# Kernel tuning notes

Hardware: AMD Instinct MI355X
Metric: run time of the kernel (lower is better)

Reference implementation:

```python
import jax, jax.numpy as jnp
import numpy as np

D = 1024
P = 4
TOP_K = 2
B = 8
LQ = 1024
LK = 1024


def setup_inputs() -> dict:
    key = jax.random.key(0)
    ks = jax.random.split(key, 16)
    s = 0.02
    inp = {
        "Q": jax.random.normal(ks[0], (B, LQ, D), jnp.float32),
        "src": jax.random.normal(ks[1], (P, B, LK, D), jnp.float32),
        # q_proj
        "Wq": jax.random.normal(ks[2], (D, D), jnp.float32) * s,
        "bq": jnp.zeros((D,), jnp.float32),
        # per-path k/v projections (stacked over paths)
        "Wk": jax.random.normal(ks[3], (P, D, D), jnp.float32) * s,
        "bk": jnp.zeros((P, D), jnp.float32),
        "Wv": jax.random.normal(ks[4], (P, D, D), jnp.float32) * s,
        "bv": jnp.zeros((P, D), jnp.float32),
        # path_score_mlp: Linear(D,D) -> ReLU -> Linear(D,P)
        "Wm1": jax.random.normal(ks[5], (D, D), jnp.float32) * s,
        "bm1": jnp.zeros((D,), jnp.float32),
        "Wm2": jax.random.normal(ks[6], (P, D), jnp.float32) * s,
        "bm2": jnp.zeros((P,), jnp.float32),
        # out_proj
        "Wo": jax.random.normal(ks[7], (D, D), jnp.float32) * s,
        "bo": jnp.zeros((D,), jnp.float32),
    }
    return inp


def reference(Q, src, Wq, bq, Wk, bk, Wv, bv, Wm1, bm1, Wm2, bm2, Wo, bo):
    # Q: [B,Lq,D], src: [P,B,Lk,D]; all Linears use torch convention y = x @ W.T + b
    d = Q.shape[-1]
    Qp = jnp.einsum("bqd,ed->bqe", Q, Wq) + bq                     # [B,Lq,D]
    K = jnp.einsum("pbkd,ped->pbke", src, Wk) + bk[:, None, None]  # [P,B,Lk,D]
    V = jnp.einsum("pbkd,ped->pbke", src, Wv) + bv[:, None, None]  # [P,B,Lk,D]
    logits = jnp.einsum("bqd,pbkd->pbqk", Qp, K) / jnp.sqrt(jnp.asarray(d, Qp.dtype))
    attn = jax.nn.softmax(logits, axis=-1)                          # [P,B,Lq,Lk]
    attn_out = jnp.einsum("pbqk,pbke->pbqe", attn, V)               # [P,B,Lq,D]

    # path gating from mean-pooled projected query
    pooled = Qp.mean(axis=1)                                        # [B,D]
    h = jax.nn.relu(pooled @ Wm1.T + bm1)
    path_logits = h @ Wm2.T + bm2                                   # [B,P]
    path_scores = jax.nn.softmax(path_logits, axis=-1)
    _, topk_idx = jax.lax.top_k(path_scores, TOP_K)                 # [B,top_k]
    mask = jax.nn.one_hot(topk_idx, P, dtype=path_scores.dtype).sum(axis=1)  # [B,P]
    sparse_w = path_scores * mask
    sparse_w = sparse_w / (sparse_w.sum(axis=1, keepdims=True) + 1e-8)

    out = jnp.einsum("pbqe,bp->bqe", attn_out, sparse_w)            # [B,Lq,D]
    return jnp.einsum("bqe,de->bqd", out, Wo) + bo
```

## Files before the change

kernel.cpp:

```cpp
#include <hip/hip_runtime.h>

#define D_  1024
#define B_  8
#define P_  4
#define LQk 1024
#define LKk 1024

typedef __attribute__((ext_vector_type(8))) short bf16x8;
typedef __attribute__((ext_vector_type(4))) float f32x4;
typedef __attribute__((ext_vector_type(8))) unsigned short ushort8v;

__device__ __forceinline__ unsigned short f2bf(float f) {
  unsigned int u = __float_as_uint(f);
  u += 0x7FFFu + ((u >> 16) & 1u);
  return (unsigned short)(u >> 16);
}

__device__ __forceinline__ void gload_lds16(const void* g, void* l) {
  __builtin_amdgcn_global_load_lds(
      (const __attribute__((address_space(1))) unsigned int*)g,
      (__attribute__((address_space(3))) unsigned int*)l, 16, 0, 0);
}

__global__ __launch_bounds__(256) void convert_bf16_kernel(const float* __restrict__ in,
                                                           unsigned short* __restrict__ out) {
  long i = ((long)blockIdx.x * 256 + threadIdx.x) * 8;
  float4 v0 = *(const float4*)(in + i);
  float4 v1 = *(const float4*)(in + i + 4);
  ushort8v r;
  r[0] = f2bf(v0.x); r[1] = f2bf(v0.y); r[2] = f2bf(v0.z); r[3] = f2bf(v0.w);
  r[4] = f2bf(v1.x); r[5] = f2bf(v1.y); r[6] = f2bf(v1.z); r[7] = f2bf(v1.w);
  *(ushort8v*)(out + i) = r;
}

__global__ __launch_bounds__(256) void zero_kernel(float* __restrict__ p) {
  p[blockIdx.x * 256 + threadIdx.x] = 0.f;
}

__global__ __launch_bounds__(256) void qmean_kernel(const float* __restrict__ Q,
                                                    float* __restrict__ Qm) {
  int d = blockIdx.x * 256 + threadIdx.x;
  int b = blockIdx.y;
  int q0 = blockIdx.z * 64;
  const float* q = Q + ((long)b * LQk + q0) * D_ + d;
  float s = 0.f;
  #pragma unroll 8
  for (int i = 0; i < 64; ++i) s += q[(long)i * D_];
  atomicAdd(&Qm[b * D_ + d], s * (1.0f / 1024.0f));
}

template<int RELU>
__global__ __launch_bounds__(256) void matvec_kernel(const float* __restrict__ X,
                                                     const float* __restrict__ W,
                                                     const float* __restrict__ bias,
                                                     float* __restrict__ out) {
  int g = blockIdx.x * 4 + (threadIdx.x >> 6);
  int lane = threadIdx.x & 63;
  int b = g >> 10, e = g & 1023;
  const float* x = X + b * D_;
  const float* w = W + (long)e * D_;
  float s = 0.f;
  #pragma unroll
  for (int k = lane * 4; k < D_; k += 256) {
    float4 xv = *(const float4*)(x + k);
    float4 wv = *(const float4*)(w + k);
    s += xv.x * wv.x + xv.y * wv.y + xv.z * wv.z + xv.w * wv.w;
  }
  #pragma unroll
  for (int o = 32; o; o >>= 1) s += __shfl_xor(s, o, 64);
  if (lane == 0) {
    s += bias[e];
    if (RELU) s = fmaxf(s, 0.f);
    out[b * D_ + e] = s;
  }
}

__global__ __launch_bounds__(256) void gate_kernel(const float* __restrict__ h,
                                                   const float* __restrict__ Wm2,
                                                   const float* __restrict__ bm2,
                                                   int* __restrict__ sel,
                                                   float* __restrict__ wsel) {
  __shared__ float lg[B_][P_];
  int lane = threadIdx.x & 63, wid = threadIdx.x >> 6;
  #pragma unroll
  for (int i = 0; i < 8; ++i) {
    int pair = wid * 8 + i;
    int b = pair >> 2, p = pair & 3;
    const float* x = h + b * D_;
    const float* w = Wm2 + p * D_;
    float s = 0.f;
    for (int k = lane; k < D_; k += 64) s += x[k] * w[k];
    #pragma unroll
    for (int o = 32; o; o >>= 1) s += __shfl_xor(s, o, 64);
    if (lane == 0) lg[b][p] = s + bm2[p];
  }
  __syncthreads();
  if (threadIdx.x < B_) {
    int b = threadIdx.x;
    float v0 = lg[b][0], v1 = lg[b][1], v2 = lg[b][2], v3 = lg[b][3];
    float m = fmaxf(fmaxf(v0, v1), fmaxf(v2, v3));
    float e[4];
    e[0] = __expf(v0 - m); e[1] = __expf(v1 - m);
    e[2] = __expf(v2 - m); e[3] = __expf(v3 - m);
    float sum = e[0] + e[1] + e[2] + e[3];
    int p0 = 0;
    for (int p = 1; p < 4; ++p) if (e[p] > e[p0]) p0 = p;
    int p1 = -1;
    for (int p = 0; p < 4; ++p) { if (p == p0) continue; if (p1 < 0 || e[p] > e[p1]) p1 = p; }
    float s0 = e[p0] / sum, s1 = e[p1] / sum;
    float dn = s0 + s1 + 1e-8f;
    sel[b * 2] = p0; sel[b * 2 + 1] = p1;
    wsel[b * 2] = s0 / dn; wsel[b * 2 + 1] = s1 / dn;
  }
}

__global__ __launch_bounds__(256) void select_convert_kernel(const float* __restrict__ src,
                                                             const int* __restrict__ sel,
                                                             unsigned short* __restrict__ out) {
  int z = blockIdx.y; int b = z >> 1; int p = sel[z];
  const float* s = src + ((long)p * B_ + b) * (1024L * 1024);
  unsigned short* o = out + (long)z * (1024L * 1024);
  long i = ((long)blockIdx.x * 256 + threadIdx.x) * 8;
  float4 v0 = *(const float4*)(s + i);
  float4 v1 = *(const float4*)(s + i + 4);
  ushort8v r;
  r[0] = f2bf(v0.x); r[1] = f2bf(v0.y); r[2] = f2bf(v0.z); r[3] = f2bf(v0.w);
  r[4] = f2bf(v1.x); r[5] = f2bf(v1.y); r[6] = f2bf(v1.z); r[7] = f2bf(v1.w);
  *(ushort8v*)(o + i) = r;
}

__global__ __launch_bounds__(256) void softmax_kernel(const float* __restrict__ S,
                                                      unsigned short* __restrict__ P,
                                                      const float* __restrict__ wsel) {
  int z = blockIdx.y;
  int row = blockIdx.x * 4 + (threadIdx.x >> 6);
  int lane = threadIdx.x & 63;
  const float* s = S + ((long)z * LQk + row) * LKk;
  float4 v[4];
  #pragma unroll
  for (int i = 0; i < 4; ++i) v[i] = *(const float4*)(s + (lane + i * 64) * 4);
  float m = -1e30f;
  #pragma unroll
  for (int i = 0; i < 4; ++i)
    m = fmaxf(m, fmaxf(fmaxf(v[i].x, v[i].y), fmaxf(v[i].z, v[i].w)));
  #pragma unroll
  for (int o = 32; o; o >>= 1) m = fmaxf(m, __shfl_xor(m, o, 64));
  const float sc = 0.03125f;
  float sum = 0.f;
  #pragma unroll
  for (int i = 0; i < 4; ++i) {
    v[i].x = __expf((v[i].x - m) * sc);
    v[i].y = __expf((v[i].y - m) * sc);
    v[i].z = __expf((v[i].z - m) * sc);
    v[i].w = __expf((v[i].w - m) * sc);
    sum += v[i].x + v[i].y + v[i].z + v[i].w;
  }
  #pragma unroll
  for (int o = 32; o; o >>= 1) sum += __shfl_xor(sum, o, 64);
  float wf = wsel[z] / sum;
  unsigned short* p = P + ((long)z * LQk + row) * LKk;
  #pragma unroll
  for (int i = 0; i < 4; ++i) {
    ushort4 r;
    r.x = f2bf(v[i].x * wf); r.y = f2bf(v[i].y * wf);
    r.z = f2bf(v[i].z * wf); r.w = f2bf(v[i].w * wf);
    *(ushort4*)(p + (lane + i * 64) * 4) = r;
  }
}

template<int BIAS_MODE, int OUT_BF16, int SEL_MODE, int SPLITK2>
__global__ __launch_bounds__(256) void gemm_nt(
    const unsigned short* __restrict__ A0, long sAz, long segA,
    const unsigned short* __restrict__ B0, long sBz, long segB,
    const float* __restrict__ bias0, long sBiasz,
    void* __restrict__ C0, long sCz,
    const int* __restrict__ sel, int K) {
  __shared__ unsigned short As[128 * 32];
  __shared__ unsigned short Bs[128 * 32];
  const int z = blockIdx.z;
  const long idxA = (SEL_MODE == 1) ? sel[z] : (SEL_MODE == 3 ? (z >> 1) : z);
  const long idxB = (SEL_MODE == 2) ? sel[z] : z;
  const unsigned short* A = A0 + idxA * sAz;
  const unsigned short* B = B0 + idxB * sBz;
  const float* bias = bias0;
  if (BIAS_MODE) {
    long idxBias = (SEL_MODE == 1 || SEL_MODE == 2) ? sel[z] : z;
    bias = bias0 + idxBias * sBiasz;
  }
  const int tid = threadIdx.x;
  const int lane = tid & 63;
  const int wid = tid >> 6;
  const int wr = wid >> 1, wc = wid & 1;
  const long rowBase = (long)blockIdx.y * 128;
  const long colBase = (long)blockIdx.x * 128;

  const int strow = lane >> 2;
  const int stcol = (lane & 3) * 8;

  f32x4 acc[4][4] = {};

  const int nk = K >> 5;
  for (int kt = 0; kt < nk; ++kt) {
    const long k0 = (long)kt << 5;
    const unsigned short* Ak;
    const unsigned short* Bk;
    if (SPLITK2 && k0 >= 1024) { Ak = A + segA + (k0 - 1024); Bk = B + segB + (k0 - 1024); }
    else                       { Ak = A + k0;                 Bk = B + k0; }
    __syncthreads();
    #pragma unroll
    for (int i = 0; i < 2; ++i) {
      const int r = wid * 32 + i * 16;
      gload_lds16(Ak + (rowBase + r + strow) * 1024 + stcol, &As[r * 32]);
      gload_lds16(Bk + (colBase + r + strow) * 1024 + stcol, &Bs[r * 32]);
    }
    __syncthreads();
    bf16x8 areg[4], breg[4];
    #pragma unroll
    for (int m = 0; m < 4; ++m)
      areg[m] = *(const bf16x8*)&As[(wr * 64 + m * 16 + (lane & 15)) * 32 + (lane >> 4) * 8];
    #pragma unroll
    for (int n = 0; n < 4; ++n)
      breg[n] = *(const bf16x8*)&Bs[(wc * 64 + n * 16 + (lane & 15)) * 32 + (lane >> 4) * 8];
    #pragma unroll
    for (int m = 0; m < 4; ++m)
      #pragma unroll
      for (int n = 0; n < 4; ++n)
        acc[m][n] = __builtin_amdgcn_mfma_f32_16x16x32_bf16(areg[m], breg[n], acc[m][n], 0, 0, 0);
  }

  unsigned short* Cb = (unsigned short*)C0 + (long)z * sCz;
  float* Cf = (float*)C0 + (long)z * sCz;
  const long crow0 = rowBase + wr * 64;
  const long ccol0 = colBase + wc * 64;
  #pragma unroll
  for (int m = 0; m < 4; ++m) {
    #pragma unroll
    for (int j = 0; j < 4; ++j) {
      const long row = crow0 + m * 16 + (lane >> 4) * 4 + j;
      const float brow = (BIAS_MODE == 2) ? bias[row] : 0.f;
      #pragma unroll
      for (int n = 0; n < 4; ++n) {
        const long col = ccol0 + n * 16 + (lane & 15);
        float v = acc[m][n][j] + brow;
        if (BIAS_MODE == 1) v += bias[col];
        if (OUT_BF16) Cb[row * 1024 + col] = f2bf(v);
        else          Cf[row * 1024 + col] = v;
      }
    }
  }
}

extern "C" void kernel_launch(void* const* d_in, const int* in_sizes, int n_in,
                              void* d_out, int out_size, void* d_ws, size_t ws_size,
                              hipStream_t stream) {
  (void)in_sizes; (void)n_in; (void)out_size; (void)ws_size;
  const float* Q   = (const float*)d_in[0];
  const float* src = (const float*)d_in[1];
  const float* Wq  = (const float*)d_in[2];
  const float* bq  = (const float*)d_in[3];
  const float* Wk  = (const float*)d_in[4];
  const float* bk  = (const float*)d_in[5];
  const float* Wv  = (const float*)d_in[6];
  const float* bv  = (const float*)d_in[7];
  const float* Wm1 = (const float*)d_in[8];
  const float* bm1 = (const float*)d_in[9];
  const float* Wm2 = (const float*)d_in[10];
  const float* bm2 = (const float*)d_in[11];
  const float* Wo  = (const float*)d_in[12];
  const float* bo  = (const float*)d_in[13];
  float* out = (float*)d_out;

  char* ws = (char*)d_ws;
  const long MBb = 1024L * 1024;
  const long ME  = 1024L * 1024;
  unsigned short* Qbf   = (unsigned short*)(ws);
  unsigned short* srcbf = (unsigned short*)(ws + 16 * MBb);
  unsigned short* Wkbf  = (unsigned short*)(ws + 48 * MBb);
  unsigned short* Wvbf  = (unsigned short*)(ws + 56 * MBb);
  float*          Sbuf  = (float*)(ws);
  unsigned short* Qpbf  = (unsigned short*)(ws + 64 * MBb);
  unsigned short* Wqbf  = (unsigned short*)(ws + 80 * MBb);
  unsigned short* Wobf  = (unsigned short*)(ws + 82 * MBb);
  unsigned short* Kbf   = (unsigned short*)(ws + 84 * MBb);
  unsigned short* Vtbf  = (unsigned short*)(ws + 116 * MBb);
  unsigned short* Pbf   = (unsigned short*)(ws + 148 * MBb);
  unsigned short* AObf  = (unsigned short*)(ws + 180 * MBb);
  float* Qmean  = (float*)(ws + 196 * MBb);
  float* pooled = (float*)(ws + 196 * MBb + 32 * 1024);
  float* hbuf   = (float*)(ws + 196 * MBb + 64 * 1024);
  int*   sel    = (int*)(ws + 196 * MBb + 96 * 1024);
  float* wsel   = (float*)(ws + 196 * MBb + 96 * 1024 + 256);

  convert_bf16_kernel<<<4096, 256, 0, stream>>>(Q, Qbf);
  convert_bf16_kernel<<<512,  256, 0, stream>>>(Wq, Wqbf);
  convert_bf16_kernel<<<2048, 256, 0, stream>>>(Wk, Wkbf);
  convert_bf16_kernel<<<2048, 256, 0, stream>>>(Wv, Wvbf);
  convert_bf16_kernel<<<512,  256, 0, stream>>>(Wo, Wobf);

  zero_kernel<<<32, 256, 0, stream>>>(Qmean);
  qmean_kernel<<<dim3(4, 8, 16), 256, 0, stream>>>(Q, Qmean);
  matvec_kernel<0><<<2048, 256, 0, stream>>>(Qmean, Wq, bq, pooled);
  matvec_kernel<1><<<2048, 256, 0, stream>>>(pooled, Wm1, bm1, hbuf);
  gate_kernel<<<1, 256, 0, stream>>>(hbuf, Wm2, bm2, sel, wsel);

  select_convert_kernel<<<dim3(512, 16), 256, 0, stream>>>(src, sel, srcbf);

  gemm_nt<1,1,0,0><<<dim3(8, 64, 1), 256, 0, stream>>>(Qbf, 0, 0, Wqbf, 0, 0, bq, 0, Qpbf, 0, nullptr, 1024);
  gemm_nt<1,1,2,0><<<dim3(8, 8, 16), 256, 0, stream>>>(srcbf, ME, 0, Wkbf, ME, 0, bk, D_, Kbf, ME, sel, 1024);
  gemm_nt<2,1,1,0><<<dim3(8, 8, 16), 256, 0, stream>>>(Wvbf, ME, 0, srcbf, ME, 0, bv, D_, Vtbf, ME, sel, 1024);
  gemm_nt<0,0,3,0><<<dim3(8, 8, 16), 256, 0, stream>>>(Qpbf, ME, 0, Kbf, ME, 0, nullptr, 0, Sbuf, ME, nullptr, 1024);
  softmax_kernel<<<dim3(256, 16), 256, 0, stream>>>(Sbuf, Pbf, wsel);
  gemm_nt<0,1,0,1><<<dim3(8, 8, 8), 256, 0, stream>>>(Pbf, 2 * ME, ME, Vtbf, 2 * ME, ME, nullptr, 0, AObf, ME, nullptr, 2048);
  gemm_nt<1,0,0,0><<<dim3(8, 64, 1), 256, 0, stream>>>(AObf, 0, 0, Wobf, 0, 0, bo, 0, out, 0, nullptr, 1024);
}
```

Before: 637.1 us.

## Replace GEMM with 256x256 double-buffered, swizzled-LDS pipelined MFMA kernel

```diff
diff --git a/kernel.cpp b/kernel.cpp
--- a/kernel.cpp
+++ b/kernel.cpp
@@ -21,6 +21,8 @@
       (const __attribute__((address_space(1))) unsigned int*)g,
       (__attribute__((address_space(3))) unsigned int*)l, 16, 0, 0);
 }
+
+#define SBAR() do { __builtin_amdgcn_sched_barrier(0); __builtin_amdgcn_s_barrier(); __builtin_amdgcn_sched_barrier(0); } while (0)
 
 __global__ __launch_bounds__(256) void convert_bf16_kernel(const float* __restrict__ in,
                                                            unsigned short* __restrict__ out) {
@@ -168,80 +170,165 @@
   }
 }
 
-template<int BIAS_MODE, int OUT_BF16, int SEL_MODE, int SPLITK2>
-__global__ __launch_bounds__(256) void gemm_nt(
+template<int BIAS_MODE, int OUT_BF16, int SEL_MODE, int SPLITK2, int SWZ>
+__global__ __launch_bounds__(512, 2) void gemm256(
     const unsigned short* __restrict__ A0, long sAz, long segA,
     const unsigned short* __restrict__ B0, long sBz, long segB,
     const float* __restrict__ bias0, long sBiasz,
     void* __restrict__ C0, long sCz,
     const int* __restrict__ sel, int K) {
-  __shared__ unsigned short As[128 * 32];
-  __shared__ unsigned short Bs[128 * 32];
-  const int z = blockIdx.z;
+  __shared__ unsigned short As[2][256 * 64];
+  __shared__ unsigned short Bs[2][256 * 64];
+  const int id = blockIdx.x;
+  int tx, ty, z;
+  if (SWZ) {
+    int m = id & 7, j = id >> 3;
+    int t = j & 15;
+    z = (j >> 4) * 8 + m;
+    tx = t & 3; ty = t >> 2;
+  } else {
+    tx = id & 3; ty = id >> 2; z = 0;
+  }
   const long idxA = (SEL_MODE == 1) ? sel[z] : (SEL_MODE == 3 ? (z >> 1) : z);
   const long idxB = (SEL_MODE == 2) ? sel[z] : z;
   const unsigned short* A = A0 + idxA * sAz;
   const unsigned short* B = B0 + idxB * sBz;
   const float* bias = bias0;
-  if (BIAS_MODE) {
-    long idxBias = (SEL_MODE == 1 || SEL_MODE == 2) ? sel[z] : z;
-    bias = bias0 + idxBias * sBiasz;
-  }
-  const int tid = threadIdx.x;
-  const int lane = tid & 63;
-  const int wid = tid >> 6;
-  const int wr = wid >> 1, wc = wid & 1;
-  const long rowBase = (long)blockIdx.y * 128;
-  const long colBase = (long)blockIdx.x * 128;
-
-  const int strow = lane >> 2;
-  const int stcol = (lane & 3) * 8;
-
-  f32x4 acc[4][4] = {};
-
-  const int nk = K >> 5;
-  for (int kt = 0; kt < nk; ++kt) {
-    const long k0 = (long)kt << 5;
-    const unsigned short* Ak;
-    const unsigned short* Bk;
-    if (SPLITK2 && k0 >= 1024) { Ak = A + segA + (k0 - 1024); Bk = B + segB + (k0 - 1024); }
-    else                       { Ak = A + k0;                 Bk = B + k0; }
-    __syncthreads();
-    #pragma unroll
-    for (int i = 0; i < 2; ++i) {
-      const int r = wid * 32 + i * 16;
-      gload_lds16(Ak + (rowBase + r + strow) * 1024 + stcol, &As[r * 32]);
-      gload_lds16(Bk + (colBase + r + strow) * 1024 + stcol, &Bs[r * 32]);
+  if (BIAS_MODE) bias = bias0 + ((SEL_MODE == 1 || SEL_MODE == 2) ? (long)sel[z] : (long)z) * sBiasz;
+
+  const int tid = threadIdx.x, lane = tid & 63, wid = tid >> 6;
+  const int wr = wid >> 2, wc = wid & 3;
+  const long rowBase = (long)ty * 256, colBase = (long)tx * 256;
+
+  const int srow = lane >> 3;
+  const int sgran = ((lane & 7) ^ (lane >> 3)) * 8;
+  const int aOff = (wr * 128 + (lane & 15)) * 64;
+  const int bOff = (wc * 64 + (lane & 15)) * 64;
+  const int gk0 = ((lane >> 4) ^ (lane & 7)) * 8;
+  const int gk1 = (((lane >> 4) + 4) ^ (lane & 7)) * 8;
+
+  const int NKT = K >> 6;
+  const int T = NKT >> 1;
+
+  f32x4 acc[8][4] = {};
+
+#define STG(ISB, HALF, KT, BUF) do {                                                   \
+    if ((KT) < NKT) {                                                                  \
+      const unsigned short* gp_ = (ISB) ? B : A;                                       \
+      const long seg_ = (ISB) ? segB : segA;                                           \
+      const long kc_ = (SPLITK2 && (KT) >= 16) ? (seg_ + (long)((KT) - 16) * 64)       \
+                                               : ((long)(KT) * 64);                    \
+      const int rb_ = (HALF) * 128 + wid * 16;                                         \
+      const long gr_ = ((ISB) ? colBase : rowBase) + rb_ + srow;                       \
+      const unsigned short* g0_ = gp_ + gr_ * 1024 + kc_ + sgran;                      \
+      unsigned short* l0_ = ((ISB) ? &Bs[BUF][0] : &As[BUF][0]) + rb_ * 64;            \
+      gload_lds16(g0_, l0_);                                                           \
+      gload_lds16(g0_ + 8 * 1024, l0_ + 8 * 64);                                       \
+    }                                                                                  \
+  } while (0)
+
+#define LDA(BUF, GK, MF) (*(const bf16x8*)&As[BUF][aOff + (MF) * 1024 + (GK)])
+#define LDB(BUF, GK, NF) (*(const bf16x8*)&Bs[BUF][bOff + (NF) * 1024 + (GK)])
+
+#define MF16(AV, BV, NLO) do {                                                         \
+    __builtin_amdgcn_s_setprio(1);                                                     \
+    _Pragma("unroll")                                                                  \
+    for (int mf_ = 0; mf_ < 8; ++mf_) {                                                \
+      acc[mf_][NLO]     = __builtin_amdgcn_mfma_f32_16x16x32_bf16(AV[mf_], BV[NLO],    \
+                                                                  acc[mf_][NLO], 0, 0, 0); \
+      acc[mf_][(NLO)+1] = __builtin_amdgcn_mfma_f32_16x16x32_bf16(AV[mf_], BV[(NLO)+1],\
+                                                                  acc[mf_][(NLO)+1], 0, 0, 0); \
+    }                                                                                  \
+    __builtin_amdgcn_s_setprio(0);                                                     \
+  } while (0)
+
+  STG(0, 0, 0, 0); STG(1, 0, 0, 0); STG(0, 1, 0, 0); STG(1, 1, 0, 0);
+  STG(0, 0, 1, 1); STG(1, 0, 1, 1);
+  __builtin_amdgcn_sched_barrier(0);
+  asm volatile("s_waitcnt vmcnt(4)" ::: "memory");
+  __builtin_amdgcn_s_barrier();
+  __builtin_amdgcn_sched_barrier(0);
+
+  for (int t = 0; t < T; ++t) {
+    const int o = 2 * t + 1, n0 = 2 * t + 2, n1 = 2 * t + 3;
+    bf16x8 a0[8], a1[8], b0[4], b1[4];
+    #pragma unroll
+    for (int i = 0; i < 8; ++i) a0[i] = LDA(0, gk0, i);
+    #pragma unroll
+    for (int i = 0; i < 4; ++i) b0[i] = LDB(0, gk0, i);
+    STG(0, 1, o, 1);
+    SBAR();
+    MF16(a0, b0, 0);
+    SBAR();
+    #pragma unroll
+    for (int i = 0; i < 8; ++i) a1[i] = LDA(0, gk1, i);
+    #pragma unroll
+    for (int i = 0; i < 4; ++i) b1[i] = LDB(0, gk1, i);
+    STG(1, 1, o, 1);
+    SBAR();
+    MF16(a0, b0, 2);
+    SBAR();
+    STG(0, 0, n0, 0);
+    SBAR();
+    MF16(a1, b1, 0);
+    SBAR();
+    STG(1, 0, n0, 0);
+    SBAR();
+    MF16(a1, b1, 2);
+    __builtin_amdgcn_sched_barrier(0);
+    if (t == T - 1) { asm volatile("s_waitcnt vmcnt(0)" ::: "memory"); }
+    else            { asm volatile("s_waitcnt vmcnt(4)" ::: "memory"); }
+    __builtin_amdgcn_s_barrier();
+    __builtin_amdgcn_sched_barrier(0);
+    #pragma unroll
+    for (int i = 0; i < 8; ++i) a0[i] = LDA(1, gk0, i);
+    #pragma unroll
+    for (int i = 0; i < 4; ++i) b0[i] = LDB(1, gk0, i);
+    STG(0, 1, n0, 0);
+    SBAR();
+    MF16(a0, b0, 0);
+    SBAR();
+    #pragma unroll
+    for (int i = 0; i < 8; ++i) a1[i] = LDA(1, gk1, i);
+    #pragma unroll
+    for (int i = 0; i < 4; ++i) b1[i] = LDB(1, gk1, i);
+    STG(1, 1, n0, 0);
+    SBAR();
+    MF16(a0, b0, 2);
+    SBAR();
+    STG(0, 0, n1, 1);
+    SBAR();
+    MF16(a1, b1, 0);
+    SBAR();
+    STG(1, 0, n1, 1);
+    SBAR();
+    MF16(a1, b1, 2);
+    if (t < T - 1) {
+      __builtin_amdgcn_sched_barrier(0);
+      asm volatile("s_waitcnt vmcnt(4)" ::: "memory");
+      __builtin_amdgcn_s_barrier();
+      __builtin_amdgcn_sched_barrier(0);
     }
-    __syncthreads();
-    bf16x8 areg[4], breg[4];
-    #pragma unroll
-    for (int m = 0; m < 4; ++m)
-      areg[m] = *(const bf16x8*)&As[(wr * 64 + m * 16 + (lane & 15)) * 32 + (lane >> 4) * 8];
-    #pragma unroll
-    for (int n = 0; n < 4; ++n)
-      breg[n] = *(const bf16x8*)&Bs[(wc * 64 + n * 16 + (lane & 15)) * 32 + (lane >> 4) * 8];
-    #pragma unroll
-    for (int m = 0; m < 4; ++m)
-      #pragma unroll
-      for (int n = 0; n < 4; ++n)
-        acc[m][n] = __builtin_amdgcn_mfma_f32_16x16x32_bf16(areg[m], breg[n], acc[m][n], 0, 0, 0);
-  }
+  }
+#undef STG
+#undef LDA
+#undef LDB
+#undef MF16
 
   unsigned short* Cb = (unsigned short*)C0 + (long)z * sCz;
   float* Cf = (float*)C0 + (long)z * sCz;
-  const long crow0 = rowBase + wr * 64;
+  const long crow0 = rowBase + wr * 128;
   const long ccol0 = colBase + wc * 64;
   #pragma unroll
-  for (int m = 0; m < 4; ++m) {
+  for (int mf = 0; mf < 8; ++mf) {
     #pragma unroll
     for (int j = 0; j < 4; ++j) {
-      const long row = crow0 + m * 16 + (lane >> 4) * 4 + j;
+      const long row = crow0 + mf * 16 + (lane >> 4) * 4 + j;
       const float brow = (BIAS_MODE == 2) ? bias[row] : 0.f;
       #pragma unroll
-      for (int n = 0; n < 4; ++n) {
-        const long col = ccol0 + n * 16 + (lane & 15);
-        float v = acc[m][n][j] + brow;
+      for (int nf = 0; nf < 4; ++nf) {
+        const long col = ccol0 + nf * 16 + (lane & 15);
+        float v = acc[mf][nf][j] + brow;
         if (BIAS_MODE == 1) v += bias[col];
         if (OUT_BF16) Cb[row * 1024 + col] = f2bf(v);
         else          Cf[row * 1024 + col] = v;
@@ -305,11 +392,11 @@
 
   select_convert_kernel<<<dim3(512, 16), 256, 0, stream>>>(src, sel, srcbf);
 
-  gemm_nt<1,1,0,0><<<dim3(8, 64, 1), 256, 0, stream>>>(Qbf, 0, 0, Wqbf, 0, 0, bq, 0, Qpbf, 0, nullptr, 1024);
-  gemm_nt<1,1,2,0><<<dim3(8, 8, 16), 256, 0, stream>>>(srcbf, ME, 0, Wkbf, ME, 0, bk, D_, Kbf, ME, sel, 1024);
-  gemm_nt<2,1,1,0><<<dim3(8, 8, 16), 256, 0, stream>>>(Wvbf, ME, 0, srcbf, ME, 0, bv, D_, Vtbf, ME, sel, 1024);
-  gemm_nt<0,0,3,0><<<dim3(8, 8, 16), 256, 0, stream>>>(Qpbf, ME, 0, Kbf, ME, 0, nullptr, 0, Sbuf, ME, nullptr, 1024);
+  gemm256<1,1,0,0,0><<<128, 512, 0, stream>>>(Qbf, 0, 0, Wqbf, 0, 0, bq, 0, Qpbf, 0, nullptr, 1024);
+  gemm256<1,1,2,0,1><<<256, 512, 0, stream>>>(srcbf, ME, 0, Wkbf, ME, 0, bk, D_, Kbf, ME, sel, 1024);
+  gemm256<2,1,1,0,1><<<256, 512, 0, stream>>>(Wvbf, ME, 0, srcbf, ME, 0, bv, D_, Vtbf, ME, sel, 1024);
+  gemm256<0,0,3,0,1><<<256, 512, 0, stream>>>(Qpbf, ME, 0, Kbf, ME, 0, nullptr, 0, Sbuf, ME, nullptr, 1024);
   softmax_kernel<<<dim3(256, 16), 256, 0, stream>>>(Sbuf, Pbf, wsel);
-  gemm_nt<0,1,0,1><<<dim3(8, 8, 8), 256, 0, stream>>>(Pbf, 2 * ME, ME, Vtbf, 2 * ME, ME, nullptr, 0, AObf, ME, nullptr, 2048);
-  gemm_nt<1,0,0,0><<<dim3(8, 64, 1), 256, 0, stream>>>(AObf, 0, 0, Wobf, 0, 0, bo, 0, out, 0, nullptr, 1024);
-}
+  gemm256<0,1,0,1,1><<<128, 512, 0, stream>>>(Pbf, 2 * ME, ME, Vtbf, 2 * ME, ME, nullptr, 0, AObf, ME, nullptr, 2048);
+  gemm256<1,0,0,0,0><<<128, 512, 0, stream>>>(AObf, 0, 0, Wobf, 0, 0, bo, 0, out, 0, nullptr, 1024);
+}
```

After: 621.5 us. 2.5% less time.
